# Kernel optimization log

Measured on AMD Instinct MI355X. Metric: run time of the kernel, lower is better.

The kernel has to match this reference:

```python
import jax, jax.numpy as jnp
import numpy as np

N_NODES = 100000
N_FEAT = 256
OUT_DIM = 128
NNZ_X = 1_600_000
NNZ_A = 1_600_000
DROPOUT = 0.0  # layer default; floor(1-p+u) mask is all-ones -> deterministic


def setup_inputs() -> dict:
    key = jax.random.key(0)
    k = jax.random.split(key, 7)
    feat_rows = jax.random.randint(k[0], (NNZ_X,), 0, N_NODES, dtype=jnp.int32)
    feat_cols = jax.random.randint(k[1], (NNZ_X,), 0, N_FEAT, dtype=jnp.int32)
    feat_vals = jax.random.normal(k[2], (NNZ_X,), dtype=jnp.float32)
    adj_rows = jax.random.randint(k[3], (NNZ_A,), 0, N_NODES, dtype=jnp.int32)
    adj_cols = jax.random.randint(k[4], (NNZ_A,), 0, N_NODES, dtype=jnp.int32)
    adj_vals = jax.random.uniform(k[5], (NNZ_A,), dtype=jnp.float32)
    glorot_std = np.sqrt(2.0 / (N_FEAT + OUT_DIM)).astype(np.float32)
    W = jax.random.normal(k[6], (N_FEAT, OUT_DIM), dtype=jnp.float32) * glorot_std
    return {
        "feat_rows": feat_rows, "feat_cols": feat_cols, "feat_vals": feat_vals,
        "adj_rows": adj_rows, "adj_cols": adj_cols, "adj_vals": adj_vals,
        "W": W, "n_nodes": N_NODES,
    }


def reference(feat_rows, feat_cols, feat_vals, adj_rows, adj_cols, adj_vals, W, n_nodes):
    # sparse dropout on feature nonzeros: mask = floor((1-p) + uniform) in {0,1}
    u = jax.random.uniform(jax.random.key(1), feat_vals.shape, dtype=feat_vals.dtype)
    keep = jnp.floor((1.0 - DROPOUT) + u)
    vals = feat_vals * keep * (1.0 / (1.0 - DROPOUT))
    # X @ W : gather W rows by feature column, scale by nnz value, scatter-add into node rows
    xw = jax.ops.segment_sum(vals[:, None] * W[feat_cols], feat_rows,
                             num_segments=n_nodes)  # [N, D]
    # A @ (X @ W) : gather node rows by edge source, scale by edge weight, scatter-add to dest
    agg = jax.ops.segment_sum(adj_vals[:, None] * xw[adj_cols], adj_rows,
                              num_segments=n_nodes)  # [N, D]
    return jax.nn.relu(agg)
```

## Files before the change

### kernel.cpp

```cpp
#include <hip/hip_runtime.h>
#include <hip/hip_fp16.h>

#define OUT_DIM 128
#define NPS 256
#define NS_MAX 400
#define CAP_S 4608
#define CURSTR 32
#define SBLK1 1024
#define EPT1 4
#define CHUNK1 (SBLK1 * EPT1)
#define SBLK2 1024
#define EPT2 5
#define GBLK 256

__global__ __launch_bounds__(SBLK1) void scatter1_kernel(
    const int* __restrict__ adj_rows, const int* __restrict__ adj_cols,
    const float* __restrict__ adj_vals, int nnz_a, int nCkA,
    const int* __restrict__ feat_rows, const int* __restrict__ feat_cols,
    const float* __restrict__ feat_vals, int nnz_x,
    int* __restrict__ cur, int2* __restrict__ pay, int ns)
{
    __shared__ int2 s_stage[CHUNK1];
    __shared__ unsigned short s_bin[CHUNK1];
    __shared__ int s_hist[NS_MAX];
    __shared__ int s_excl[NS_MAX];
    __shared__ int s_gbase[NS_MAX];

    int tid = threadIdx.x;
    bool isA = ((int)blockIdx.x < nCkA);
    const int* rows; const int* cols; const float* vals;
    int nnz, start, matbase;
    if (isA) {
        rows = adj_rows; cols = adj_cols; vals = adj_vals; nnz = nnz_a;
        start = (int)blockIdx.x * CHUNK1; matbase = 0;
    } else {
        rows = feat_rows; cols = feat_cols; vals = feat_vals; nnz = nnz_x;
        start = ((int)blockIdx.x - nCkA) * CHUNK1; matbase = ns;
    }
    int total = nnz - start; if (total > CHUNK1) total = CHUNK1;

    for (int i = tid; i < ns; i += SBLK1) s_hist[i] = 0;
    __syncthreads();

    int rr[EPT1]; int cc[EPT1]; float vv[EPT1];
    #pragma unroll
    for (int k = 0; k < EPT1; ++k) {
        int e = start + k * SBLK1 + tid;
        rr[k] = -1;
        if (e < nnz) {
            rr[k] = rows[e]; cc[k] = cols[e]; vv[k] = vals[e];
            atomicAdd(&s_hist[rr[k] >> 8], 1);
        }
    }
    __syncthreads();

    if (tid < 64) {
        int carry = 0;
        for (int seg = 0; seg < ns; seg += 64) {
            int idx = seg + tid;
            int x = (idx < ns) ? s_hist[idx] : 0;
            int incl = x;
            #pragma unroll
            for (int off = 1; off < 64; off <<= 1) {
                int y = __shfl_up(incl, off, 64);
                if (tid >= off) incl += y;
            }
            if (idx < ns) s_excl[idx] = carry + incl - x;
            carry += __shfl(incl, 63, 64);
        }
    }
    __syncthreads();

    for (int i = tid; i < ns; i += SBLK1) {
        int c = s_hist[i];
        s_gbase[i] = (c > 0) ? atomicAdd(&cur[(matbase + i) * CURSTR], c) : 0;
        s_hist[i] = 0;
    }
    __syncthreads();

    #pragma unroll
    for (int k = 0; k < EPT1; ++k) {
        if (rr[k] >= 0) {
            int b = rr[k] >> 8;
            int rl = rr[k] & 255;
            int pos = s_excl[b] + atomicAdd(&s_hist[b], 1);
            s_stage[pos] = make_int2((rl << 17) | cc[k], __float_as_int(vv[k]));
            s_bin[pos] = (unsigned short)b;
        }
    }
    __syncthreads();

    for (int i = tid; i < total; i += SBLK1) {
        int b = s_bin[i];
        int g = s_gbase[b] + (i - s_excl[b]);
        if (g < CAP_S)
            pay[(size_t)(matbase + b) * CAP_S + g] = s_stage[i];
    }
}

__device__ __forceinline__ void sort2_body(
    const int* __restrict__ cur, int2* __restrict__ pay,
    int2* __restrict__ row_span, int b, int ns, int n_nodes)
{
    __shared__ int s_cnt[NPS];
    __shared__ int s_excl[NPS];
    int tid = threadIdx.x;
    int count = cur[b * CURSTR]; if (count > CAP_S) count = CAP_S;
    int2* region = pay + (size_t)b * CAP_S;

    if (tid < NPS) s_cnt[tid] = 0;
    __syncthreads();

    int2 er[EPT2];
    #pragma unroll
    for (int k = 0; k < EPT2; ++k) {
        int i = tid + k * SBLK2;
        er[k] = make_int2(-1, 0);
        if (i < count) {
            er[k] = region[i];
            atomicAdd(&s_cnt[((unsigned)er[k].x) >> 17], 1);
        }
    }
    __syncthreads();

    if (tid < 64) {
        int carry = 0;
        #pragma unroll
        for (int seg = 0; seg < NPS; seg += 64) {
            int x = s_cnt[seg + tid];
            int incl = x;
            #pragma unroll
            for (int off = 1; off < 64; off <<= 1) {
                int y = __shfl_up(incl, off, 64);
                if (tid >= off) incl += y;
            }
            s_excl[seg + tid] = carry + incl - x;
            carry += __shfl(incl, 63, 64);
        }
    }
    __syncthreads();

    int m = (b >= ns) ? 1 : 0;
    if (tid < NPS) {
        int g = (b - m * ns) * NPS + tid;
        if (g < n_nodes)
            row_span[(size_t)m * n_nodes + g] =
                make_int2(b * CAP_S + s_excl[tid], s_cnt[tid]);
    }
    __syncthreads();

    #pragma unroll
    for (int k = 0; k < EPT2; ++k) {
        if (er[k].x >= 0) {
            int rl = ((unsigned)er[k].x) >> 17;
            int pos = atomicAdd(&s_excl[rl], 1);
            region[pos] = make_int2(er[k].x & 0x1FFFF, er[k].y);
        }
    }
}

__global__ __launch_bounds__(SBLK2) void sort2x_kernel(
    const int* __restrict__ cur, int2* __restrict__ pay,
    int2* __restrict__ row_span, int ns, int n_nodes)
{
    sort2_body(cur, pay, row_span, ns + blockIdx.x, ns, n_nodes);
}

__global__ void wcast_kernel(const float* __restrict__ W, __half* __restrict__ W16, int n) {
    int i = blockIdx.x * blockDim.x + threadIdx.x;
    if (i < n) W16[i] = __float2half(W[i]);
}

__global__ __launch_bounds__(SBLK2) void sortA_xw_kernel(
    const int* __restrict__ cur, int2* __restrict__ pay,
    int2* __restrict__ row_span,
    const __half* __restrict__ W16, __half* __restrict__ XW,
    int ns, int n_nodes)
{
    if ((int)blockIdx.x < ns) {
        sort2_body(cur, pay, row_span, blockIdx.x, ns, n_nodes);
        return;
    }
    int tid = threadIdx.x;
    int lane = tid & 15;
    int node = ((int)blockIdx.x - ns) * 64 + (tid >> 4);
    if (node >= n_nodes) return;
    int2 span = row_span[(size_t)n_nodes + node];
    int s = span.x, cnt = span.y;
    const int4* Wv = (const int4*)W16;
    float a0=0,a1=0,a2=0,a3=0,a4=0,a5=0,a6=0,a7=0;
    for (int base = 0; base < cnt; base += 16) {
        int mm = cnt - base; if (mm > 16) mm = 16;
        int2 pl = make_int2(0, 0);
        if (lane < mm) pl = pay[s + base + lane];
        #pragma unroll 4
        for (int j = 0; j < mm; ++j) {
            int c = __shfl(pl.x, j, 16);
            float v = __int_as_float(__shfl(pl.y, j, 16));
            union { int4 i4; __half2 h[4]; } u;
            u.i4 = Wv[(size_t)c * 16 + lane];
            float2 f0 = __half22float2(u.h[0]);
            float2 f1 = __half22float2(u.h[1]);
            float2 f2 = __half22float2(u.h[2]);
            float2 f3 = __half22float2(u.h[3]);
            a0 += v * f0.x; a1 += v * f0.y; a2 += v * f1.x; a3 += v * f1.y;
            a4 += v * f2.x; a5 += v * f2.y; a6 += v * f3.x; a7 += v * f3.y;
        }
    }
    union { int4 i4; __half2 h[4]; } o;
    o.h[0] = __floats2half2_rn(a0, a1);
    o.h[1] = __floats2half2_rn(a2, a3);
    o.h[2] = __floats2half2_rn(a4, a5);
    o.h[3] = __floats2half2_rn(a6, a7);
    ((int4*)(XW + (size_t)node * OUT_DIM))[lane] = o.i4;
}

__global__ __launch_bounds__(GBLK, 4) void gather_agg_kernel(
    const int2* __restrict__ row_span, const int2* __restrict__ pay,
    const __half* __restrict__ XW, float* __restrict__ out, int n_nodes)
{
    int tid = threadIdx.x;
    int lane = tid & 15;
    int node = blockIdx.x * 16 + (tid >> 4);
    if (node >= n_nodes) return;
    int2 span = row_span[node];
    int s = span.x, cnt = span.y;
    const int4* Xv = (const int4*)XW;
    float a0=0,a1=0,a2=0,a3=0,a4=0,a5=0,a6=0,a7=0;
    int2 pl = make_int2(0, 0);
    if (lane < cnt) pl = pay[s + lane];
    for (int base = 0; base < cnt; base += 16) {
        int4 w[16];
        #pragma unroll
        for (int j = 0; j < 16; ++j) {
            int c = __shfl(pl.x, j, 16);
            w[j] = Xv[(size_t)((c << 4) | lane)];
        }
        int2 pln = make_int2(0, 0);
        if (base + 16 + lane < cnt) pln = pay[s + base + 16 + lane];
        #pragma unroll
        for (int j = 0; j < 16; ++j) {
            float v = __int_as_float(__shfl(pl.y, j, 16));
            union { int4 i4; __half2 h[4]; } u;
            u.i4 = w[j];
            float2 f0 = __half22float2(u.h[0]);
            float2 f1 = __half22float2(u.h[1]);
            float2 f2 = __half22float2(u.h[2]);
            float2 f3 = __half22float2(u.h[3]);
            a0 += v * f0.x; a1 += v * f0.y; a2 += v * f1.x; a3 += v * f1.y;
            a4 += v * f2.x; a5 += v * f2.y; a6 += v * f3.x; a7 += v * f3.y;
        }
        pl = pln;
    }
    float4 lo, hi;
    lo.x = fmaxf(a0, 0.f); lo.y = fmaxf(a1, 0.f);
    lo.z = fmaxf(a2, 0.f); lo.w = fmaxf(a3, 0.f);
    hi.x = fmaxf(a4, 0.f); hi.y = fmaxf(a5, 0.f);
    hi.z = fmaxf(a6, 0.f); hi.w = fmaxf(a7, 0.f);
    float4* orow = (float4*)(out + (size_t)node * OUT_DIM);
    orow[2 * lane]     = lo;
    orow[2 * lane + 1] = hi;
}

extern "C" void kernel_launch(void* const* d_in, const int* in_sizes, int n_in,
                              void* d_out, int out_size, void* d_ws, size_t ws_size,
                              hipStream_t stream) {
    const int*   feat_rows = (const int*)d_in[0];
    const int*   feat_cols = (const int*)d_in[1];
    const float* feat_vals = (const float*)d_in[2];
    const int*   adj_rows  = (const int*)d_in[3];
    const int*   adj_cols  = (const int*)d_in[4];
    const float* adj_vals  = (const float*)d_in[5];
    const float* W         = (const float*)d_in[6];
    float*       out       = (float*)d_out;

    const int nnz_x   = in_sizes[0];
    const int nnz_a   = in_sizes[3];
    const int n_w     = in_sizes[6];
    const int n_nodes = out_size / OUT_DIM;
    const int ns      = (n_nodes + NPS - 1) / NPS;

    char* p = (char*)d_ws;
    __half* XW   = (__half*)p;  p += (size_t)n_nodes * OUT_DIM * sizeof(__half);
    __half* W16  = (__half*)p;  p += (size_t)n_w * sizeof(__half);
    p = (char*)(((uintptr_t)p + 127) & ~(uintptr_t)127);
    int2* pay    = (int2*)p;    p += (size_t)2 * ns * CAP_S * sizeof(int2);
    int2* row_span = (int2*)p;  p += (size_t)2 * n_nodes * sizeof(int2);
    p = (char*)(((uintptr_t)p + 127) & ~(uintptr_t)127);
    int* cur     = (int*)p;     p += (size_t)2 * ns * CURSTR * sizeof(int);

    (void)hipMemsetAsync(cur, 0, (size_t)2 * ns * CURSTR * sizeof(int), stream);

    wcast_kernel<<<(n_w + 255) / 256, 256, 0, stream>>>(W, W16, n_w);

    const int nCkA = (nnz_a + CHUNK1 - 1) / CHUNK1;
    const int nCkX = (nnz_x + CHUNK1 - 1) / CHUNK1;
    scatter1_kernel<<<nCkA + nCkX, SBLK1, 0, stream>>>(
        adj_rows, adj_cols, adj_vals, nnz_a, nCkA,
        feat_rows, feat_cols, feat_vals, nnz_x,
        cur, pay, ns);

    sort2x_kernel<<<ns, SBLK2, 0, stream>>>(cur, pay, row_span, ns, n_nodes);

    const int gnb64 = (n_nodes + 63) / 64;
    sortA_xw_kernel<<<ns + gnb64, SBLK2, 0, stream>>>(
        cur, pay, row_span, W16, XW, ns, n_nodes);

    const int gnb = (n_nodes + 15) / 16;
    gather_agg_kernel<<<gnb, GBLK, 0, stream>>>(row_span, pay, XW, out, n_nodes);
}
```

Before: 234.4 us.

## Overlap adjacency scatter with feature-bucket sort in one launch

The combined scatter kernel is split so the feature-matrix scatter runs first on its own. The adjacency scatter then shares a launch with the per-bucket sort of the feature entries, which only depends on the earlier feature scatter. This removes one kernel boundary and lets the adjacency scatter overlap with the X-side sort instead of running serialized. Both bodies now share one kernel, so the union of their shared-memory allocations may lower occupancy, and the sort half now uses SBLK1 launch bounds.

Result: no change. 235.2 us (+0.3%).

```diff
diff --git a/kernel.cpp b/kernel.cpp
--- a/kernel.cpp
+++ b/kernel.cpp
@@ -13,12 +13,10 @@
 #define EPT2 5
 #define GBLK 256
 
-__global__ __launch_bounds__(SBLK1) void scatter1_kernel(
-    const int* __restrict__ adj_rows, const int* __restrict__ adj_cols,
-    const float* __restrict__ adj_vals, int nnz_a, int nCkA,
-    const int* __restrict__ feat_rows, const int* __restrict__ feat_cols,
-    const float* __restrict__ feat_vals, int nnz_x,
-    int* __restrict__ cur, int2* __restrict__ pay, int ns)
+__device__ __forceinline__ void scatter1_body(
+    const int* __restrict__ rows, const int* __restrict__ cols,
+    const float* __restrict__ vals, int nnz, int chunk,
+    int* __restrict__ cur, int2* __restrict__ pay, int ns, int matbase)
 {
     __shared__ int2 s_stage[CHUNK1];
     __shared__ unsigned short s_bin[CHUNK1];
@@ -27,16 +25,7 @@
     __shared__ int s_gbase[NS_MAX];
 
     int tid = threadIdx.x;
-    bool isA = ((int)blockIdx.x < nCkA);
-    const int* rows; const int* cols; const float* vals;
-    int nnz, start, matbase;
-    if (isA) {
-        rows = adj_rows; cols = adj_cols; vals = adj_vals; nnz = nnz_a;
-        start = (int)blockIdx.x * CHUNK1; matbase = 0;
-    } else {
-        rows = feat_rows; cols = feat_cols; vals = feat_vals; nnz = nnz_x;
-        start = ((int)blockIdx.x - nCkA) * CHUNK1; matbase = ns;
-    }
+    int start = chunk * CHUNK1;
     int total = nnz - start; if (total > CHUNK1) total = CHUNK1;
 
     for (int i = tid; i < ns; i += SBLK1) s_hist[i] = 0;
@@ -98,12 +87,20 @@
     }
 }
 
+__global__ __launch_bounds__(SBLK1) void scatter1x_kernel(
+    const int* __restrict__ rows, const int* __restrict__ cols,
+    const float* __restrict__ vals, int nnz,
+    int* __restrict__ cur, int2* __restrict__ pay, int ns)
+{
+    scatter1_body(rows, cols, vals, nnz, blockIdx.x, cur, pay, ns, ns);
+}
+
 __device__ __forceinline__ void sort2_body(
     const int* __restrict__ cur, int2* __restrict__ pay,
     int2* __restrict__ row_span, int b, int ns, int n_nodes)
 {
     __shared__ int s_cnt[NPS];
-    __shared__ int s_excl[NPS];
+    __shared__ int s_excl2[NPS];
     int tid = threadIdx.x;
     int count = cur[b * CURSTR]; if (count > CAP_S) count = CAP_S;
     int2* region = pay + (size_t)b * CAP_S;
@@ -134,7 +131,7 @@
                 int y = __shfl_up(incl, off, 64);
                 if (tid >= off) incl += y;
             }
-            s_excl[seg + tid] = carry + incl - x;
+            s_excl2[seg + tid] = carry + incl - x;
             carry += __shfl(incl, 63, 64);
         }
     }
@@ -145,7 +142,7 @@
         int g = (b - m * ns) * NPS + tid;
         if (g < n_nodes)
             row_span[(size_t)m * n_nodes + g] =
-                make_int2(b * CAP_S + s_excl[tid], s_cnt[tid]);
+                make_int2(b * CAP_S + s_excl2[tid], s_cnt[tid]);
     }
     __syncthreads();
 
@@ -153,17 +150,24 @@
     for (int k = 0; k < EPT2; ++k) {
         if (er[k].x >= 0) {
             int rl = ((unsigned)er[k].x) >> 17;
-            int pos = atomicAdd(&s_excl[rl], 1);
+            int pos = atomicAdd(&s_excl2[rl], 1);
             region[pos] = make_int2(er[k].x & 0x1FFFF, er[k].y);
         }
     }
 }
 
-__global__ __launch_bounds__(SBLK2) void sort2x_kernel(
-    const int* __restrict__ cur, int2* __restrict__ pay,
+__global__ __launch_bounds__(SBLK1) void scA_s2x_kernel(
+    const int* __restrict__ adj_rows, const int* __restrict__ adj_cols,
+    const float* __restrict__ adj_vals, int nnz_a, int nCkA,
+    int* __restrict__ cur, int2* __restrict__ pay,
     int2* __restrict__ row_span, int ns, int n_nodes)
 {
-    sort2_body(cur, pay, row_span, ns + blockIdx.x, ns, n_nodes);
+    if ((int)blockIdx.x < nCkA) {
+        scatter1_body(adj_rows, adj_cols, adj_vals, nnz_a, blockIdx.x,
+                      cur, pay, ns, 0);
+    } else {
+        sort2_body(cur, pay, row_span, ns + ((int)blockIdx.x - nCkA), ns, n_nodes);
+    }
 }
 
 __global__ void wcast_kernel(const float* __restrict__ W, __half* __restrict__ W16, int n) {
@@ -295,12 +299,13 @@
 
     const int nCkA = (nnz_a + CHUNK1 - 1) / CHUNK1;
     const int nCkX = (nnz_x + CHUNK1 - 1) / CHUNK1;
-    scatter1_kernel<<<nCkA + nCkX, SBLK1, 0, stream>>>(
+
+    scatter1x_kernel<<<nCkX, SBLK1, 0, stream>>>(
+        feat_rows, feat_cols, feat_vals, nnz_x, cur, pay, ns);
+
+    scA_s2x_kernel<<<nCkA + ns, SBLK1, 0, stream>>>(
         adj_rows, adj_cols, adj_vals, nnz_a, nCkA,
-        feat_rows, feat_cols, feat_vals, nnz_x,
-        cur, pay, ns);
-
-    sort2x_kernel<<<ns, SBLK2, 0, stream>>>(cur, pay, row_span, ns, n_nodes);
+        cur, pay, row_span, ns, n_nodes);
 
     const int gnb64 = (n_nodes + 63) / 64;
     sortA_xw_kernel<<<ns + gnb64, SBLK2, 0, stream>>>(
```
